# Optimization experiments

Measured on AMD Instinct MI355X. Metric: run time of the kernel, lower is better.

Reference implementation:

```python
import jax, jax.numpy as jnp
import numpy as np

B, H, W = 16, 64, 64
C_IN, C_OUT, W_DIM = 256, 128, 128


def modulated_conv2d(x, kernel, style):
    """StyleGAN2 modulated+demodulated conv, vmapped over batch.
    x: [B,H,W,C_in], kernel: [kH,kW,C_in,C_out], style: [B,C_in]."""
    kH = kernel.shape[0]
    pad = kH // 2

    def conv_single(x_i, s_i):
        kern = kernel * s_i[None, None, :, None]
        denom = jnp.sqrt(jnp.sum(kern ** 2, axis=(0, 1, 2), keepdims=True) + 1e-08)
        kern = kern / denom
        return jax.lax.conv_general_dilated(
            x_i[None], kern, window_strides=(1, 1),
            padding=((pad, pad), (pad, pad)),
            dimension_numbers=('NHWC', 'HWIO', 'NHWC'))[0]

    return jax.vmap(conv_single)(x, style)


def pixel_shuffle(x, scale=2):
    b, h, w, c = x.shape
    s = scale
    c_out = c // (s * s)
    x = x.reshape(b, h, w, s, s, c_out)
    x = x.transpose(0, 1, 3, 2, 4, 5)
    return x.reshape(b, h * s, w * s, c_out)


def setup_inputs() -> dict:
    key = jax.random.key(0)
    ks = jax.random.split(key, 12)
    dense_std = 1.0 / np.sqrt(W_DIM)  # lecun_normal-like for Dense
    return {
        'x': jax.random.normal(ks[0], (B, H, W, C_IN), jnp.float32),
        'w': jax.random.normal(ks[1], (B, W_DIM), jnp.float32),
        'affine1_w': jax.random.normal(ks[2], (W_DIM, C_IN), jnp.float32) * dense_std,
        'affine1_b': jnp.ones((C_IN,), jnp.float32),  # bias_init=ones
        'kernel1': jax.random.normal(ks[3], (3, 3, C_IN, C_IN), jnp.float32),
        'noise_scale1': jnp.full((1,), 0.1, jnp.float32),
        'bias1': jax.random.normal(ks[4], (C_IN,), jnp.float32) * 0.02,
        'affine2_w': jax.random.normal(ks[5], (W_DIM, C_IN), jnp.float32) * dense_std,
        'affine2_b': jnp.ones((C_IN,), jnp.float32),
        'kernel2': jax.random.normal(ks[6], (3, 3, C_IN, C_OUT * 4), jnp.float32),
        'noise_scale2': jnp.full((1,), 0.1, jnp.float32),
        'bias2': jax.random.normal(ks[7], (C_OUT * 4,), jnp.float32) * 0.02,
        'noise1': jax.random.normal(ks[8], (B, H, W, 1), jnp.float32),
        'noise2': jax.random.normal(ks[9], (B, H, W, 1), jnp.float32),
    }


def reference(x, w, affine1_w, affine1_b, kernel1, noise_scale1, bias1,
              affine2_w, affine2_b, kernel2, noise_scale2, bias2,
              noise1, noise2):
    # style affine 1 -> modulated conv (C_in -> C_in)
    s1 = w @ affine1_w + affine1_b                      # [B, C_in]
    h = modulated_conv2d(x, kernel1, s1)                # [B,H,W,C_in]
    h = h + noise1 * noise_scale1
    h = jax.nn.leaky_relu(h + bias1, negative_slope=0.2)
    # style affine 2 -> modulated conv (C_in -> 4*C_out)
    s2 = w @ affine2_w + affine2_b                      # [B, C_in]
    h = modulated_conv2d(h, kernel2, s2)                # [B,H,W,4*C_out]
    h = h + noise2 * noise_scale2
    h = jax.nn.leaky_relu(h + bias2, negative_slope=0.2)
    return pixel_shuffle(h, scale=2)                    # [B,2H,2W,C_out]
```

## Files before the change

### kernel.cpp

```cpp
#include <hip/hip_runtime.h>
#include <type_traits>


#define CIN 256

typedef _Float16 half4 __attribute__((ext_vector_type(4)));
typedef _Float16 half8 __attribute__((ext_vector_type(8)));
typedef float f32x4 __attribute__((ext_vector_type(4)));

__global__ __launch_bounds__(256) void style_kernel(
    const float* __restrict__ w, const float* __restrict__ a1w, const float* __restrict__ a1b,
    const float* __restrict__ a2w, const float* __restrict__ a2b,
    float* __restrict__ s1, float* __restrict__ s2)
{
  const int b = blockIdx.x, c = threadIdx.x;
  const float* wb = w + b * 128;
  float acc1 = 0.f, acc2 = 0.f;
  for (int k = 0; k < 128; ++k) {
    const float wv = wb[k];
    acc1 = fmaf(wv, a1w[k * 256 + c], acc1);
    acc2 = fmaf(wv, a2w[k * 256 + c], acc2);
  }
  s1[b * 256 + c] = acc1 + a1b[c];
  s2[b * 256 + c] = acc2 + a2b[c];
}

__global__ __launch_bounds__(256) void ksq_kernel(
    const float* __restrict__ kern, float* __restrict__ ksq, int n)
{
  const int i = blockIdx.x * 256 + threadIdx.x;
  if (i < n) {
    float acc = 0.f;
    for (int t = 0; t < 9; ++t) { const float v = kern[t * n + i]; acc = fmaf(v, v, acc); }
    ksq[i] = acc;
  }
}

__global__ __launch_bounds__(256) void demod_kernel(
    const float* __restrict__ s, const float* __restrict__ ksq,
    float* __restrict__ demod, int cout)
{
  const int b = blockIdx.y;
  const int o = blockIdx.x * 256 + threadIdx.x;
  const float* sb = s + b * 256;
  float acc = 1e-8f;
  for (int i = 0; i < 256; ++i) {
    const float sv = sb[i];
    acc = fmaf(sv * sv, ksq[i * cout + o], acc);
  }
  demod[b * cout + o] = 1.0f / sqrtf(acc);
}

__global__ __launch_bounds__(256) void kprep_kernel(
    const float* __restrict__ Kw, _Float16* __restrict__ Bt, int cout)
{
  __shared__ float T[64][68];
  const int tap = blockIdx.z;
  const int o0 = blockIdx.x * 64, c0 = blockIdx.y * 64;
  const int t = threadIdx.x;
  #pragma unroll
  for (int it = 0; it < 4; ++it) {
    const int c = (t >> 4) + it * 16;
    const int o = (t & 15) * 4;
    *(float4*)(&T[c][o]) = *(const float4*)(Kw + ((size_t)tap * CIN + c0 + c) * cout + o0 + o);
  }
  __syncthreads();
  #pragma unroll
  for (int it = 0; it < 4; ++it) {
    const int o = (t >> 4) + it * 16;
    const int c = (t & 15) * 4;
    half4 hv = {(_Float16)T[c][o], (_Float16)T[c + 1][o],
                (_Float16)T[c + 2][o], (_Float16)T[c + 3][o]};
    *(half4*)(&Bt[((size_t)tap * cout + o0 + o) * CIN + c0 + c]) = hv;
  }
}

template <int COUT, bool AMOD, bool SHUFFLE, typename TIN, typename TOUT>
__global__ __launch_bounds__(512) void conv_mfma(
    const TIN* __restrict__ X,
    const float* __restrict__ Sg,
    const _Float16* __restrict__ Bt,
    const float* __restrict__ D,
    const float* __restrict__ NZ,
    const float* __restrict__ NSp,
    const float* __restrict__ BIAS,
    const float* __restrict__ SMOD,
    TOUT* __restrict__ OUT)
{
  __shared__ __align__(16) _Float16 As[66][72];
  __shared__ __align__(16) _Float16 Bs[3][128][72];

  const int t = threadIdx.x;
  constexpr int nwg = (COUT / 128) * 1024;
  constexpr int q = nwg >> 3;
  const int lin = blockIdx.x;
  const int wgid = (lin & 7) * q + (lin >> 3);
  const int row = wgid & 1023, oc = wgid >> 10;
  const int b = row >> 6, y = row & 63;
  const int o0 = oc * 128;

  const int lane = t & 63, wid = t >> 6;
  const int wm = wid & 1, wn = wid >> 1;
  const int lrow = lane >> 4;
  const int lcol = lane & 15;

  const int sr = t >> 3;
  const int sco = (t & 7) * 8;

  f32x4 acc[2][2];
  #pragma unroll
  for (int m = 0; m < 2; ++m)
    #pragma unroll
    for (int n = 0; n < 2; ++n)
      acc[m][n] = (f32x4){0.f, 0.f, 0.f, 0.f};

  const TIN* Xb = X + (size_t)b * (64 * 64 * 256);

  for (int dyi = 0; dyi < 3; ++dyi) {
    const int ys = y + dyi - 1;
    const bool vrow = ((unsigned)ys < 64u);
    const TIN* Xrow = Xb + (size_t)(vrow ? ys : 0) * (64 * 256);

    for (int c0 = 0; c0 < 256; c0 += 64) {
      __syncthreads();
      #pragma unroll
      for (int part = 0; part < 2; ++part) {
        const int r = part ? 64 + (t >> 3) : sr;
        if (part == 0 || t < 16) {
          const int xs = r - 1;
          const bool v = vrow && ((unsigned)xs < 64u);
          half8 hv = {(_Float16)0, (_Float16)0, (_Float16)0, (_Float16)0,
                      (_Float16)0, (_Float16)0, (_Float16)0, (_Float16)0};
          if (v) {
            if constexpr (AMOD) {
              const float4 x0 = *(const float4*)(Xrow + (size_t)xs * 256 + c0 + sco);
              const float4 x1 = *(const float4*)(Xrow + (size_t)xs * 256 + c0 + sco + 4);
              const float4 s0 = *(const float4*)(Sg + b * 256 + c0 + sco);
              const float4 s1v = *(const float4*)(Sg + b * 256 + c0 + sco + 4);
              hv[0] = (_Float16)(x0.x * s0.x);  hv[1] = (_Float16)(x0.y * s0.y);
              hv[2] = (_Float16)(x0.z * s0.z);  hv[3] = (_Float16)(x0.w * s0.w);
              hv[4] = (_Float16)(x1.x * s1v.x); hv[5] = (_Float16)(x1.y * s1v.y);
              hv[6] = (_Float16)(x1.z * s1v.z); hv[7] = (_Float16)(x1.w * s1v.w);
            } else {
              hv = *(const half8*)(Xrow + (size_t)xs * 256 + c0 + sco);
            }
          }
          *(half8*)(&As[r][sco]) = hv;
        }
      }
      #pragma unroll
      for (int dxi = 0; dxi < 3; ++dxi) {
        const int tap = dyi * 3 + dxi;
        const _Float16* Bsrc = Bt + ((size_t)tap * COUT + o0) * 256 + c0;
        #pragma unroll
        for (int pass = 0; pass < 2; ++pass) {
          const int n = (t >> 3) + pass * 64;
          *(half8*)(&Bs[dxi][n][sco]) = *(const half8*)(Bsrc + (size_t)n * 256 + sco);
        }
      }
      __syncthreads();
      #pragma unroll
      for (int dxi = 0; dxi < 3; ++dxi) {
        const int abase = dxi + wm * 32 + lcol;
        #pragma unroll
        for (int ks = 0; ks < 2; ++ks) {
          const int ko = ks * 32 + lrow * 8;
          const half8 a0 = *(const half8*)(&As[abase][ko]);
          const half8 a1 = *(const half8*)(&As[abase + 16][ko]);
          const half8 b0 = *(const half8*)(&Bs[dxi][wn * 32 + lcol][ko]);
          const half8 b1 = *(const half8*)(&Bs[dxi][wn * 32 + 16 + lcol][ko]);
          acc[0][0] = __builtin_amdgcn_mfma_f32_16x16x32_f16(a0, b0, acc[0][0], 0, 0, 0);
          acc[0][1] = __builtin_amdgcn_mfma_f32_16x16x32_f16(a0, b1, acc[0][1], 0, 0, 0);
          acc[1][0] = __builtin_amdgcn_mfma_f32_16x16x32_f16(a1, b0, acc[1][0], 0, 0, 0);
          acc[1][1] = __builtin_amdgcn_mfma_f32_16x16x32_f16(a1, b1, acc[1][1], 0, 0, 0);
        }
      }
    }
  }

  const float ns = NSp[0];
  #pragma unroll
  for (int n = 0; n < 2; ++n) {
    const int o = o0 + wn * 32 + n * 16 + lcol;
    const float dmv = D[b * COUT + o];
    const float bv = BIAS[o];
    float smv = 1.0f;
    if constexpr (!SHUFFLE) smv = SMOD[b * 256 + o];
    #pragma unroll
    for (int m = 0; m < 2; ++m) {
      #pragma unroll
      for (int r = 0; r < 4; ++r) {
        const int p = wm * 32 + m * 16 + lrow * 4 + r;
        const float nzv = NZ[(size_t)(b * 64 + y) * 64 + p] * ns;
        float v = fmaf(acc[m][n][r], dmv, nzv + bv);
        v = fmaxf(v, 0.2f * v);
        if constexpr (!SHUFFLE) {
          OUT[((size_t)(b * 64 + y) * 64 + p) * COUT + o] = (TOUT)(v * smv);
        } else {
          const int g = o >> 7, c = o & 127;
          const int sh = g >> 1, sw = g & 1;
          OUT[(((size_t)(b * 128) + 2 * y + sh) * 128 + (2 * p + sw)) * 128 + c] = (TOUT)v;
        }
      }
    }
  }
}

extern "C" void kernel_launch(void* const* d_in, const int* in_sizes, int n_in,
                              void* d_out, int out_size, void* d_ws, size_t ws_size,
                              hipStream_t stream)
{
  const float* x   = (const float*)d_in[0];
  const float* w   = (const float*)d_in[1];
  const float* a1w = (const float*)d_in[2];
  const float* a1b = (const float*)d_in[3];
  const float* k1  = (const float*)d_in[4];
  const float* ns1 = (const float*)d_in[5];
  const float* b1  = (const float*)d_in[6];
  const float* a2w = (const float*)d_in[7];
  const float* a2b = (const float*)d_in[8];
  const float* k2  = (const float*)d_in[9];
  const float* ns2 = (const float*)d_in[10];
  const float* b2  = (const float*)d_in[11];
  const float* nz1 = (const float*)d_in[12];
  const float* nz2 = (const float*)d_in[13];
  float* out = (float*)d_out;

  float* ws = (float*)d_ws;
  float* s1   = ws;
  float* s2   = ws + 4096;
  float* ksq1 = ws + 8192;
  float* ksq2 = ws + 73728;
  float* dm1  = ws + 204800;
  float* dm2  = ws + 208896;
  _Float16* Bt1 = (_Float16*)(ws + 217088);
  _Float16* Bt2 = Bt1 + 9 * 256 * 256;
  _Float16* h2m = Bt2 + 9 * 512 * 256;

  style_kernel<<<16, 256, 0, stream>>>(w, a1w, a1b, a2w, a2b, s1, s2);
  ksq_kernel<<<65536 / 256, 256, 0, stream>>>(k1, ksq1, 65536);
  ksq_kernel<<<131072 / 256, 256, 0, stream>>>(k2, ksq2, 131072);
  demod_kernel<<<dim3(1, 16), 256, 0, stream>>>(s1, ksq1, dm1, 256);
  demod_kernel<<<dim3(2, 16), 256, 0, stream>>>(s2, ksq2, dm2, 512);
  kprep_kernel<<<dim3(4, 4, 9), 256, 0, stream>>>(k1, Bt1, 256);
  kprep_kernel<<<dim3(8, 4, 9), 256, 0, stream>>>(k2, Bt2, 512);

  conv_mfma<256, true, false, float, _Float16><<<2048, 512, 0, stream>>>(
      x, s1, Bt1, dm1, nz1, ns1, b1, s2, h2m);
  conv_mfma<512, false, true, _Float16, float><<<4096, 512, 0, stream>>>(
      h2m, nullptr, Bt2, dm2, nz2, ns2, b2, nullptr, out);
}
```

Measured before the change: 582.1 us.

## Restructure conv into per-row blocks with register-held weight fragments and prescaled input

The fp32 input modulation moves into a separate xprep kernel that writes prescaled fp16 activations. Each conv block now handles a whole image row across all output channels, with one wave per 128 channels. Weight fragments are loaded straight from global memory into registers instead of being staged in LDS. A full 256-channel input row goes into LDS once per dy, which cuts barriers and lets each wave reuse A fragments across 8 N tiles. The cost is a large accumulator set (128 floats per lane), fewer blocks and threads, and higher register pressure that may limit occupancy or cause spills.

```diff
diff --git a/kernel.cpp b/kernel.cpp
--- a/kernel.cpp
+++ b/kernel.cpp
@@ -1,8 +1,5 @@
 #include <hip/hip_runtime.h>
-#include <type_traits>
-
-
-#define CIN 256
+
 
 typedef _Float16 half4 __attribute__((ext_vector_type(4)));
 typedef _Float16 half8 __attribute__((ext_vector_type(8)));
@@ -62,7 +59,7 @@
   for (int it = 0; it < 4; ++it) {
     const int c = (t >> 4) + it * 16;
     const int o = (t & 15) * 4;
-    *(float4*)(&T[c][o]) = *(const float4*)(Kw + ((size_t)tap * CIN + c0 + c) * cout + o0 + o);
+    *(float4*)(&T[c][o]) = *(const float4*)(Kw + ((size_t)tap * 256 + c0 + c) * cout + o0 + o);
   }
   __syncthreads();
   #pragma unroll
@@ -71,135 +68,130 @@
     const int c = (t & 15) * 4;
     half4 hv = {(_Float16)T[c][o], (_Float16)T[c + 1][o],
                 (_Float16)T[c + 2][o], (_Float16)T[c + 3][o]};
-    *(half4*)(&Bt[((size_t)tap * cout + o0 + o) * CIN + c0 + c]) = hv;
-  }
-}
-
-template <int COUT, bool AMOD, bool SHUFFLE, typename TIN, typename TOUT>
-__global__ __launch_bounds__(512) void conv_mfma(
-    const TIN* __restrict__ X,
-    const float* __restrict__ Sg,
+    *(half4*)(&Bt[((size_t)tap * cout + o0 + o) * 256 + c0 + c]) = hv;
+  }
+}
+
+__global__ __launch_bounds__(256) void xprep_kernel(
+    const float* __restrict__ X, const float* __restrict__ S, _Float16* __restrict__ O)
+{
+  const int i = blockIdx.x * 256 + threadIdx.x;
+  const int b = i >> 17;
+  const int c8 = (i & 31) * 8;
+  const float4 x0 = *(const float4*)(X + (size_t)i * 8);
+  const float4 x1 = *(const float4*)(X + (size_t)i * 8 + 4);
+  const float4 s0 = *(const float4*)(S + b * 256 + c8);
+  const float4 s1v = *(const float4*)(S + b * 256 + c8 + 4);
+  half8 hv;
+  hv[0] = (_Float16)(x0.x * s0.x);  hv[1] = (_Float16)(x0.y * s0.y);
+  hv[2] = (_Float16)(x0.z * s0.z);  hv[3] = (_Float16)(x0.w * s0.w);
+  hv[4] = (_Float16)(x1.x * s1v.x); hv[5] = (_Float16)(x1.y * s1v.y);
+  hv[6] = (_Float16)(x1.z * s1v.z); hv[7] = (_Float16)(x1.w * s1v.w);
+  *(half8*)(&O[(size_t)i * 8]) = hv;
+}
+
+template <int COUT, bool SHUFFLE, int NTHR>
+__global__ __launch_bounds__(NTHR, 2) void conv_mfma(
+    const _Float16* __restrict__ X,
     const _Float16* __restrict__ Bt,
     const float* __restrict__ D,
     const float* __restrict__ NZ,
     const float* __restrict__ NSp,
     const float* __restrict__ BIAS,
     const float* __restrict__ SMOD,
-    TOUT* __restrict__ OUT)
-{
-  __shared__ __align__(16) _Float16 As[66][72];
-  __shared__ __align__(16) _Float16 Bs[3][128][72];
+    void* __restrict__ OUTv)
+{
+  __shared__ __align__(16) _Float16 As[66][264];
 
   const int t = threadIdx.x;
-  constexpr int nwg = (COUT / 128) * 1024;
-  constexpr int q = nwg >> 3;
   const int lin = blockIdx.x;
-  const int wgid = (lin & 7) * q + (lin >> 3);
-  const int row = wgid & 1023, oc = wgid >> 10;
-  const int b = row >> 6, y = row & 63;
-  const int o0 = oc * 128;
-
-  const int lane = t & 63, wid = t >> 6;
-  const int wm = wid & 1, wn = wid >> 1;
-  const int lrow = lane >> 4;
-  const int lcol = lane & 15;
-
-  const int sr = t >> 3;
-  const int sco = (t & 7) * 8;
-
-  f32x4 acc[2][2];
-  #pragma unroll
-  for (int m = 0; m < 2; ++m)
+  const int wgid = (lin & 7) * 128 + (lin >> 3);
+  const int b = wgid >> 6, y = wgid & 63;
+
+  const int lane = t & 63, wn = t >> 6;
+  const int lrow = lane >> 4, lcol = lane & 15;
+  const int o0w = wn * 128;
+
+  f32x4 acc[4][8];
+  #pragma unroll
+  for (int m = 0; m < 4; ++m)
     #pragma unroll
-    for (int n = 0; n < 2; ++n)
+    for (int n = 0; n < 8; ++n)
       acc[m][n] = (f32x4){0.f, 0.f, 0.f, 0.f};
 
-  const TIN* Xb = X + (size_t)b * (64 * 64 * 256);
+  const int scol = (t & 31) * 8;
 
   for (int dyi = 0; dyi < 3; ++dyi) {
     const int ys = y + dyi - 1;
     const bool vrow = ((unsigned)ys < 64u);
-    const TIN* Xrow = Xb + (size_t)(vrow ? ys : 0) * (64 * 256);
-
-    for (int c0 = 0; c0 < 256; c0 += 64) {
-      __syncthreads();
-      #pragma unroll
-      for (int part = 0; part < 2; ++part) {
-        const int r = part ? 64 + (t >> 3) : sr;
-        if (part == 0 || t < 16) {
-          const int xs = r - 1;
-          const bool v = vrow && ((unsigned)xs < 64u);
-          half8 hv = {(_Float16)0, (_Float16)0, (_Float16)0, (_Float16)0,
-                      (_Float16)0, (_Float16)0, (_Float16)0, (_Float16)0};
-          if (v) {
-            if constexpr (AMOD) {
-              const float4 x0 = *(const float4*)(Xrow + (size_t)xs * 256 + c0 + sco);
-              const float4 x1 = *(const float4*)(Xrow + (size_t)xs * 256 + c0 + sco + 4);
-              const float4 s0 = *(const float4*)(Sg + b * 256 + c0 + sco);
-              const float4 s1v = *(const float4*)(Sg + b * 256 + c0 + sco + 4);
-              hv[0] = (_Float16)(x0.x * s0.x);  hv[1] = (_Float16)(x0.y * s0.y);
-              hv[2] = (_Float16)(x0.z * s0.z);  hv[3] = (_Float16)(x0.w * s0.w);
-              hv[4] = (_Float16)(x1.x * s1v.x); hv[5] = (_Float16)(x1.y * s1v.y);
-              hv[6] = (_Float16)(x1.z * s1v.z); hv[7] = (_Float16)(x1.w * s1v.w);
-            } else {
-              hv = *(const half8*)(Xrow + (size_t)xs * 256 + c0 + sco);
-            }
-          }
-          *(half8*)(&As[r][sco]) = hv;
-        }
-      }
-      #pragma unroll
-      for (int dxi = 0; dxi < 3; ++dxi) {
-        const int tap = dyi * 3 + dxi;
-        const _Float16* Bsrc = Bt + ((size_t)tap * COUT + o0) * 256 + c0;
+    const _Float16* Xrow = X + (((size_t)(b * 64 + (vrow ? ys : 0))) * 64) * 256;
+
+    __syncthreads();
+    for (int r = (t >> 5); r < 66; r += (NTHR >> 5)) {
+      const int xs = r - 1;
+      half8 hv = {};
+      if (vrow && (unsigned)xs < 64u)
+        hv = *(const half8*)(Xrow + (size_t)xs * 256 + scol);
+      *(half8*)(&As[r][scol]) = hv;
+    }
+    __syncthreads();
+
+    for (int dxi = 0; dxi < 3; ++dxi) {
+      const _Float16* Bp = Bt + ((size_t)(dyi * 3 + dxi) * COUT + o0w) * 256
+                         + (size_t)lcol * 256 + lrow * 8;
+      #pragma unroll 1
+      for (int c0 = 0; c0 < 256; c0 += 64) {
+        half8 bf[8][2];
         #pragma unroll
-        for (int pass = 0; pass < 2; ++pass) {
-          const int n = (t >> 3) + pass * 64;
-          *(half8*)(&Bs[dxi][n][sco]) = *(const half8*)(Bsrc + (size_t)n * 256 + sco);
-        }
-      }
-      __syncthreads();
-      #pragma unroll
-      for (int dxi = 0; dxi < 3; ++dxi) {
-        const int abase = dxi + wm * 32 + lcol;
+        for (int n = 0; n < 8; ++n)
+          #pragma unroll
+          for (int ks = 0; ks < 2; ++ks)
+            bf[n][ks] = *(const half8*)(Bp + (size_t)n * 16 * 256 + c0 + ks * 32);
+        half8 af[4][2];
         #pragma unroll
-        for (int ks = 0; ks < 2; ++ks) {
-          const int ko = ks * 32 + lrow * 8;
-          const half8 a0 = *(const half8*)(&As[abase][ko]);
-          const half8 a1 = *(const half8*)(&As[abase + 16][ko]);
-          const half8 b0 = *(const half8*)(&Bs[dxi][wn * 32 + lcol][ko]);
-          const half8 b1 = *(const half8*)(&Bs[dxi][wn * 32 + 16 + lcol][ko]);
-          acc[0][0] = __builtin_amdgcn_mfma_f32_16x16x32_f16(a0, b0, acc[0][0], 0, 0, 0);
-          acc[0][1] = __builtin_amdgcn_mfma_f32_16x16x32_f16(a0, b1, acc[0][1], 0, 0, 0);
-          acc[1][0] = __builtin_amdgcn_mfma_f32_16x16x32_f16(a1, b0, acc[1][0], 0, 0, 0);
-          acc[1][1] = __builtin_amdgcn_mfma_f32_16x16x32_f16(a1, b1, acc[1][1], 0, 0, 0);
-        }
+        for (int m = 0; m < 4; ++m)
+          #pragma unroll
+          for (int ks = 0; ks < 2; ++ks)
+            af[m][ks] = *(const half8*)(&As[dxi + m * 16 + lcol][c0 + ks * 32 + lrow * 8]);
+        #pragma unroll
+        for (int ks = 0; ks < 2; ++ks)
+          #pragma unroll
+          for (int m = 0; m < 4; ++m)
+            #pragma unroll
+            for (int n = 0; n < 8; ++n)
+              acc[m][n] = __builtin_amdgcn_mfma_f32_16x16x32_f16(af[m][ks], bf[n][ks], acc[m][n], 0, 0, 0);
       }
     }
   }
 
   const float ns = NSp[0];
-  #pragma unroll
-  for (int n = 0; n < 2; ++n) {
-    const int o = o0 + wn * 32 + n * 16 + lcol;
+  float nzv[4][4];
+  #pragma unroll
+  for (int m = 0; m < 4; ++m)
+    #pragma unroll
+    for (int rr = 0; rr < 4; ++rr)
+      nzv[m][rr] = NZ[(size_t)(b * 64 + y) * 64 + m * 16 + lrow * 4 + rr] * ns;
+
+  #pragma unroll
+  for (int n = 0; n < 8; ++n) {
+    const int o = o0w + n * 16 + lcol;
     const float dmv = D[b * COUT + o];
     const float bv = BIAS[o];
     float smv = 1.0f;
     if constexpr (!SHUFFLE) smv = SMOD[b * 256 + o];
     #pragma unroll
-    for (int m = 0; m < 2; ++m) {
+    for (int m = 0; m < 4; ++m) {
       #pragma unroll
-      for (int r = 0; r < 4; ++r) {
-        const int p = wm * 32 + m * 16 + lrow * 4 + r;
-        const float nzv = NZ[(size_t)(b * 64 + y) * 64 + p] * ns;
-        float v = fmaf(acc[m][n][r], dmv, nzv + bv);
+      for (int rr = 0; rr < 4; ++rr) {
+        const int p = m * 16 + lrow * 4 + rr;
+        float v = fmaf(acc[m][n][rr], dmv, nzv[m][rr] + bv);
         v = fmaxf(v, 0.2f * v);
         if constexpr (!SHUFFLE) {
-          OUT[((size_t)(b * 64 + y) * 64 + p) * COUT + o] = (TOUT)(v * smv);
+          ((_Float16*)OUTv)[((size_t)(b * 64 + y) * 64 + p) * COUT + o] = (_Float16)(v * smv);
         } else {
-          const int g = o >> 7, c = o & 127;
-          const int sh = g >> 1, sw = g & 1;
-          OUT[(((size_t)(b * 128) + 2 * y + sh) * 128 + (2 * p + sw)) * 128 + c] = (TOUT)v;
+          const int c = n * 16 + lcol;
+          const int sh = wn >> 1, sw = wn & 1;
+          ((float*)OUTv)[(((size_t)(b * 128) + 2 * y + sh) * 128 + (2 * p + sw)) * 128 + c] = v;
         }
       }
     }
@@ -236,6 +228,7 @@
   _Float16* Bt1 = (_Float16*)(ws + 217088);
   _Float16* Bt2 = Bt1 + 9 * 256 * 256;
   _Float16* h2m = Bt2 + 9 * 512 * 256;
+  _Float16* x1m = h2m + 16 * 64 * 64 * 256;
 
   style_kernel<<<16, 256, 0, stream>>>(w, a1w, a1b, a2w, a2b, s1, s2);
   ksq_kernel<<<65536 / 256, 256, 0, stream>>>(k1, ksq1, 65536);
@@ -244,9 +237,10 @@
   demod_kernel<<<dim3(2, 16), 256, 0, stream>>>(s2, ksq2, dm2, 512);
   kprep_kernel<<<dim3(4, 4, 9), 256, 0, stream>>>(k1, Bt1, 256);
   kprep_kernel<<<dim3(8, 4, 9), 256, 0, stream>>>(k2, Bt2, 512);
-
-  conv_mfma<256, true, false, float, _Float16><<<2048, 512, 0, stream>>>(
-      x, s1, Bt1, dm1, nz1, ns1, b1, s2, h2m);
-  conv_mfma<512, false, true, _Float16, float><<<4096, 512, 0, stream>>>(
-      h2m, nullptr, Bt2, dm2, nz2, ns2, b2, nullptr, out);
-}
+  xprep_kernel<<<8192, 256, 0, stream>>>(x, s1, x1m);
+
+  conv_mfma<256, false, 128><<<1024, 128, 0, stream>>>(
+      x1m, Bt1, dm1, nz1, ns1, b1, s2, (void*)h2m);
+  conv_mfma<512, true, 256><<<1024, 256, 0, stream>>>(
+      h2m, Bt2, dm2, nz2, ns2, b2, nullptr, (void*)out);
+}
```

Result: slower. 674.1 us (+15.8%).
